# Kernel tuning notes

Measured on AMD Instinct MI355X. Metric: run time of the kernel, lower is better.

## Reference

```python
import jax, jax.numpy as jnp
import numpy as np

B, N, D, H = 8, 1024, 512, 8
DK = D // H  # key_dim == val_dim == 64
LN_EPS = 1e-5


def setup_inputs() -> dict:
    key = jax.random.key(0)
    ks = jax.random.split(key, 16)
    stdv = 1.0 / np.sqrt(D)
    u = lambda k, shape, s: jax.random.uniform(k, shape, jnp.float32, -s, s)
    inp = {
        'q': jax.random.normal(ks[0], (B, N, D), jnp.float32),
        'mask': jax.random.uniform(ks[1], (B, N, N)) < 0.1,  # True = masked out
        # eps1 is torch.zeros in the source (never re-initialized); use small
        'eps1': jax.random.normal(ks[2], (D, D), jnp.float32) * 0.03,
        # 3 MLP layers, stacked on leading axis. Linear: y = x @ W.T + b
        'U_w': u(ks[3], (3, D, D), stdv), 'U_b': u(ks[4], (3, D), stdv),
        'V_w': u(ks[5], (3, D, D), stdv), 'V_b': u(ks[6], (3, D), stdv),
        'ln_g': jnp.ones((3, D), jnp.float32), 'ln_b': jnp.zeros((3, D), jnp.float32),
        'W_query': u(ks[7], (H, D, DK), 1.0 / np.sqrt(DK)),
        'W_key':   u(ks[8], (H, D, DK), 1.0 / np.sqrt(DK)),
        'W_val':   u(ks[9], (H, D, DK), 1.0 / np.sqrt(DK)),
        'W_out':   u(ks[10], (H, DK, D), stdv),
    }
    return inp


def _layer_norm(x, g, b):
    mu = jnp.mean(x, axis=-1, keepdims=True)
    var = jnp.mean(jnp.square(x - mu), axis=-1, keepdims=True)
    return (x - mu) * jax.lax.rsqrt(var + LN_EPS) * g + b


def _mlp_layer(x, Uw, Ub, Vw, Vb, g, b):
    # U1 -> (identity maxpool k=1) -> V1 -> LayerNorm -> ReLU -> residual
    y = x @ Uw.T + Ub
    y = y @ Vw.T + Vb
    y = _layer_norm(y, g, b)
    return x + jax.nn.relu(y)


def reference(q, mask, eps1, U_w, U_b, V_w, V_b, ln_g, ln_b,
              W_query, W_key, W_val, W_out):
    nf = 1.0 / np.sqrt(DK)  # norm_factor; applied to BOTH Q and K as in source
    h = q
    for l in range(3):
        h = _mlp_layer(h @ eps1, U_w[l], U_b[l], V_w[l], V_b[l], ln_g[l], ln_b[l])
    # per-head projections: (H,B,N,DK)
    Q = jnp.einsum('bqd,hdk->hbqk', q, W_query) * nf
    K = jnp.einsum('bgd,hdk->hbgk', h, W_key) * nf
    V = jnp.einsum('bgd,hdk->hbgk', h, W_val)
    scores = jnp.einsum('hbqk,hbgk->hbqg', Q, K)  # (H,B,N,N)
    scores = jnp.where(mask[None], -1e10, scores)
    attn = jax.nn.softmax(scores, axis=-1)
    heads = jnp.einsum('hbqg,hbgv->hbqv', attn, V)
    out = jnp.einsum('hbqv,hvd->bqd', heads, W_out)  # (B,N,D)
    return out
```

## Files before the change

kernel.cpp:

```cpp
#include <hip/hip_runtime.h>

typedef __attribute__((ext_vector_type(8))) short bhalf8;
typedef __attribute__((ext_vector_type(4))) short bhalf4;
typedef __attribute__((ext_vector_type(4))) float f32x4;

__device__ __forceinline__ ushort f2bf(float f) {
  unsigned u = __builtin_bit_cast(unsigned, f);
  unsigned r = u + 0x7fffu + ((u >> 16) & 1u);
  return (ushort)(r >> 16);
}

__device__ __forceinline__ void gld16(const ushort* g, ushort* l) {
  __builtin_amdgcn_global_load_lds((const __attribute__((address_space(1))) void*)g,
                                   (__attribute__((address_space(3))) void*)l, 16, 0, 0);
}

__global__ __launch_bounds__(256) void prep_kernel(
    const float* __restrict__ q, const int* __restrict__ mask,
    const float* __restrict__ eps1, const float* __restrict__ U_w,
    const float* __restrict__ V_w, const float* __restrict__ Wq,
    const float* __restrict__ Wk, const float* __restrict__ Wv,
    const float* __restrict__ Wo, const float* __restrict__ U_b,
    const float* __restrict__ V_b,
    ushort* __restrict__ qb, unsigned long long* __restrict__ minv,
    ushort* __restrict__ uwb, ushort* __restrict__ vwb,
    ushort* __restrict__ e1b, ushort* __restrict__ e1t,
    ushort* __restrict__ wqkv, ushort* __restrict__ wot,
    float* __restrict__ cvec) {
  int i = blockIdx.x * 256 + threadIdx.x;
  if (i < 4194304) {
    qb[i] = f2bf(q[i]);
  } else if (i < 12582912) {
    int j = i - 4194304;
    unsigned long long bb = __ballot(mask[j] != 0);
    if ((threadIdx.x & 63) == 0) {
      int b = j >> 20, qq = (j >> 10) & 1023, g = j & 1023;
      minv[((size_t)b * 16 + (g >> 6)) * 1024 + qq] = ~bb;
    }
  } else if (i < 13369344) {
    int j = i - 12582912;
    uwb[j] = f2bf(U_w[j]);
  } else if (i < 14155776) {
    int j = i - 13369344;
    vwb[j] = f2bf(V_w[j]);
  } else if (i < 14417920) {
    int j = i - 14155776;
    e1b[j] = f2bf(eps1[j]);
  } else if (i < 14680064) {
    int j = i - 14417920; int n = j >> 9, k = j & 511;
    e1t[j] = f2bf(eps1[k * 512 + n]);
  } else if (i < 15466496) {
    int j = i - 14680064; int n = j >> 9, d = j & 511;
    const float* W = (n < 512) ? Wq : (n < 1024 ? Wk : Wv);
    float sc = (n < 512) ? 0.02255252509f : 1.0f;
    int nl = n & 511;
    wqkv[j] = f2bf(W[((nl >> 6) * 512 + d) * 64 + (nl & 63)] * sc);
  } else if (i < 15728640) {
    int j = i - 15466496; int d = j >> 9, hv = j & 511;
    wot[j] = f2bf(Wo[hv * 512 + d]);
  } else {
    int j = i - 15728640;
    int idx = j >> 6, ln = j & 63;
    int l = idx >> 9;
    const float* vr = V_w + (size_t)idx * 512 + ln * 8;
    const float* ur = U_b + l * 512 + ln * 8;
    float s = 0;
#pragma unroll
    for (int t = 0; t < 8; t++) s += vr[t] * ur[t];
#pragma unroll
    for (int off = 1; off < 64; off <<= 1) s += __shfl_xor(s, off, 64);
    if (ln == 0) cvec[idx] = s + V_b[idx];
  }
}

template <int BN>
__global__ __launch_bounds__(256) void gemm_nt(
    const ushort* __restrict__ A0, const ushort* __restrict__ A1,
    const ushort* __restrict__ Bt0, const ushort* __restrict__ Bt1,
    int bsplit, int mstride, int M, int K,
    ushort* __restrict__ Oa, const float* __restrict__ ba, int ca,
    ushort* __restrict__ Ob, const float* __restrict__ bb2, int cb,
    ushort* __restrict__ Oc, const float* __restrict__ bc, int cc) {
  __shared__ ushort As[128 * 32];
  __shared__ ushort Bs[BN * 32];
  int tid = threadIdx.x;
  int wave = tid >> 6, lane = tid & 63;
  int quad = lane >> 4, col = lane & 15;
  int m0 = blockIdx.x * 128, n0 = blockIdx.y * BN;
  const ushort* A = (A1 && n0 >= 512) ? A1 : A0;
  const ushort* Bp = ((n0 < bsplit) ? Bt0 + (size_t)n0 * K
                                    : Bt1 + (size_t)(n0 - bsplit) * K) +
                     (size_t)(m0 >> 9) * mstride;
  constexpr int NI = BN / 32;
  int wm = (BN == 128) ? (wave >> 1) * 64 : (wave & 1) * 64;
  int wn = (BN == 128) ? (wave & 1) * 64 : (wave >> 1) * 32;
  f32x4 acc[4][NI] = {};
  int srow = wave * 16 + (lane >> 2);
  int skc = (lane & 3) * 8;
  const ushort* gA0 = A + (size_t)(m0 + srow) * K + skc;
  const ushort* gA1 = gA0 + (size_t)64 * K;
  const ushort* gB0 = Bp + (size_t)srow * K + skc;
  const ushort* gB1 = gB0 + (size_t)64 * K;
  ushort* lA0 = &As[wave * 16 * 32];
  ushort* lA1 = &As[(64 + wave * 16) * 32];
  ushort* lB0 = &Bs[wave * 16 * 32];
  ushort* lB1 = (BN == 128) ? &Bs[(64 + wave * 16) * 32] : nullptr;

  gld16(gA0, lA0);
  gld16(gA1, lA1);
  gld16(gB0, lB0);
  if (BN == 128) gld16(gB1, lB1);

  for (int k0 = 0; k0 < K; k0 += 32) {
    __syncthreads();
    bhalf8 af[4], bg[NI];
#pragma unroll
    for (int i = 0; i < 4; i++)
      af[i] = *(bhalf8*)&As[(wm + i * 16 + col) * 32 + quad * 8];
#pragma unroll
    for (int i = 0; i < NI; i++)
      bg[i] = *(bhalf8*)&Bs[(wn + i * 16 + col) * 32 + quad * 8];
    __syncthreads();
    if (k0 + 32 < K) {
      gld16(gA0 + k0 + 32, lA0);
      gld16(gA1 + k0 + 32, lA1);
      gld16(gB0 + k0 + 32, lB0);
      if (BN == 128) gld16(gB1 + k0 + 32, lB1);
    }
#pragma unroll
    for (int mi = 0; mi < 4; mi++)
#pragma unroll
      for (int ni = 0; ni < NI; ni++)
        acc[mi][ni] = __builtin_amdgcn_mfma_f32_16x16x32_bf16(af[mi], bg[ni], acc[mi][ni], 0, 0, 0);
  }

  int reg = n0 >> 9;
  ushort* O = (reg == 0) ? Oa : (reg == 1 ? Ob : Oc);
  const float* bs = (reg == 0) ? ba : (reg == 1 ? bb2 : bc);
  int code = (reg == 0) ? ca : (reg == 1 ? cb : cc);
#pragma unroll
  for (int mi = 0; mi < 4; mi++)
#pragma unroll
    for (int ni = 0; ni < NI; ni++) {
      int cn = n0 + wn + ni * 16 + col;
      int cnl = cn & 511;
      int cmb = m0 + wm + mi * 16 + quad * 4;
      float bv = bs ? bs[cnl] : 0.f;
      if (code == 2) {
        int bhh = (cmb >> 10) * 8 + (cnl >> 6);
        size_t base = ((size_t)bhh * 64 + ((cmb & 1023) >> 4)) * 1024 +
                      (size_t)((cnl >> 5) & 1) * 512 + (size_t)(cmb & 15) * 32 + (cnl & 31);
#pragma unroll
        for (int r = 0; r < 4; r++)
          O[base + r * 32] = f2bf(acc[mi][ni][r] + bv);
      } else if (code == 3) {
        int bhh = (cmb >> 10) * 8 + (cnl >> 6);
        size_t base = ((size_t)bhh * 64 + ((cmb & 1023) >> 4)) * 1024 +
                      (size_t)(cnl & 63) * 16 + (cmb & 15);
        ushort4 pk;
        pk.x = f2bf(acc[mi][ni][0] + bv);
        pk.y = f2bf(acc[mi][ni][1] + bv);
        pk.z = f2bf(acc[mi][ni][2] + bv);
        pk.w = f2bf(acc[mi][ni][3] + bv);
        *(ushort4*)&O[base] = pk;
      } else if (code == 1) {
        float* Ff = (float*)O;
#pragma unroll
        for (int r = 0; r < 4; r++)
          Ff[(size_t)(cmb + r) * 512 + cnl] = acc[mi][ni][r] + bv;
      } else {
#pragma unroll
        for (int r = 0; r < 4; r++)
          O[(size_t)(cmb + r) * 512 + cnl] = f2bf(acc[mi][ni][r] + bv);
      }
    }
}

__global__ __launch_bounds__(256) void ln_kernel(
    const float* __restrict__ z, const ushort* __restrict__ tb,
    const float* __restrict__ lgam, const float* __restrict__ lbet,
    ushort* __restrict__ hb) {
  int row = blockIdx.x * 4 + (threadIdx.x >> 6);
  int lane = threadIdx.x & 63;
  int cbase = lane * 8;
  const float* zr = z + (size_t)row * 512 + cbase;
  float x[8];
  *(float4*)&x[0] = *(const float4*)zr;
  *(float4*)&x[4] = *(const float4*)(zr + 4);
  float sum = 0;
#pragma unroll
  for (int i = 0; i < 8; i++) sum += x[i];
#pragma unroll
  for (int off = 1; off < 64; off <<= 1) sum += __shfl_xor(sum, off, 64);
  float mu = sum * (1.f / 512.f);
  float vs = 0;
#pragma unroll
  for (int i = 0; i < 8; i++) { float d = x[i] - mu; vs += d * d; }
#pragma unroll
  for (int off = 1; off < 64; off <<= 1) vs += __shfl_xor(vs, off, 64);
  float rstd = rsqrtf(vs * (1.f / 512.f) + 1e-5f);
  uint4 tr = *(const uint4*)&tb[(size_t)row * 512 + cbase];
  float tv[8];
  {
    const unsigned* u = (const unsigned*)&tr;
#pragma unroll
    for (int w = 0; w < 4; w++) {
      tv[2 * w] = __builtin_bit_cast(float, u[w] << 16);
      tv[2 * w + 1] = __builtin_bit_cast(float, u[w] & 0xFFFF0000u);
    }
  }
  ushort outv[8];
#pragma unroll
  for (int i = 0; i < 8; i++) {
    float val = (x[i] - mu) * rstd * lgam[cbase + i] + lbet[cbase + i];
    outv[i] = f2bf(tv[i] + fmaxf(val, 0.f));
  }
  *(uint4*)&hb[(size_t)row * 512 + cbase] = *(uint4*)outv;
}

struct KVb { bhalf8 k[4]; bhalf4 v[8]; };

__device__ __forceinline__ void ldkv(KVb& d, const ushort* kp, const ushort* vp) {
  d.k[0] = *(const bhalf8*)kp;
  d.k[1] = *(const bhalf8*)(kp + 512);
  d.k[2] = *(const bhalf8*)(kp + 1024);
  d.k[3] = *(const bhalf8*)(kp + 1536);
#pragma unroll
  for (int i = 0; i < 8; i++) d.v[i] = *(const bhalf4*)(vp + i * 256);
}

__device__ __forceinline__ void attn_step(const KVb& kv, unsigned long long m,
                                          int bs, int quad, bhalf8 bq0, bhalf8 bq1,
                                          f32x4* o, float& lsum) {
  unsigned shq = (unsigned)(m >> (bs + quad * 4));
#pragma unroll
  for (int gt = 0; gt < 2; ++gt) {
    f32x4 s = {};
    s = __builtin_amdgcn_mfma_f32_16x16x32_bf16(kv.k[2 * gt], bq0, s, 0, 0, 0);
    s = __builtin_amdgcn_mfma_f32_16x16x32_bf16(kv.k[2 * gt + 1], bq1, s, 0, 0, 0);
    unsigned pu[4];
#pragma unroll
    for (int r = 0; r < 4; ++r) {
      const int pos = gt * 16 + r;
      unsigned keep = (unsigned)((int)(shq << (31 - pos)) >> 31);
      pu[r] = __builtin_bit_cast(unsigned, __builtin_amdgcn_exp2f(s[r])) & keep;
      lsum += __builtin_bit_cast(float, pu[r]);
    }
    uint2 pp;
    pp.x = ((pu[0] + 0x8000u) >> 16) | (((pu[1] + 0x8000u) >> 16) << 16);
    pp.y = ((pu[2] + 0x8000u) >> 16) | (((pu[3] + 0x8000u) >> 16) << 16);
    bhalf4 bp = __builtin_bit_cast(bhalf4, pp);
#pragma unroll
    for (int vt = 0; vt < 4; ++vt)
      o[vt] = __builtin_amdgcn_mfma_f32_16x16x16bf16_1k(kv.v[gt * 4 + vt], bp, o[vt], 0, 0, 0);
  }
}

__global__ __launch_bounds__(256, 4) void attn_kernel(
    const ushort* __restrict__ QtT, const ushort* __restrict__ KtT,
    const ushort* __restrict__ VtT, const unsigned long long* __restrict__ minv,
    ushort* __restrict__ Op) {
  int bh = blockIdx.x;
  int b = bh >> 3, h = bh & 7;
  int tid = threadIdx.x, w = tid >> 6, lane = tid & 63;
  int quad = lane >> 4, col = lane & 15;
  int qt = blockIdx.y * 4 + w;
  const ushort* Kt = KtT + (size_t)bh * 65536 + col * 32 + quad * 8;
  const ushort* Vt = VtT + (size_t)bh * 65536 + col * 16 + quad * 4;
  const ushort* Qt = QtT + (size_t)bh * 65536 + col * 32 + quad * 8;
  bhalf8 bq0 = *(const bhalf8*)(Qt + (size_t)qt * 1024);
  bhalf8 bq1 = *(const bhalf8*)(Qt + (size_t)qt * 1024 + 512);
  f32x4 o[4] = {};
  float lsum = 0.f;
  const unsigned long long* mb = minv + (size_t)b * 16384 + qt * 16 + col;

  KVb A, Bv;
  unsigned long long mcur = mb[0], mnxt = 0;
  ldkv(A, Kt, Vt);
  for (int p = 0; p < 30; p += 2) {
    ldkv(Bv, Kt + (size_t)(p + 1) * 2048, Vt + (size_t)(p + 1) * 2048);
    mnxt = mb[((p >> 1) + 1) * 1024];
    attn_step(A, mcur, 0, quad, bq0, bq1, o, lsum);
    ldkv(A, Kt + (size_t)(p + 2) * 2048, Vt + (size_t)(p + 2) * 2048);
    attn_step(Bv, mcur, 32, quad, bq0, bq1, o, lsum);
    mcur = mnxt;
  }
  ldkv(Bv, Kt + (size_t)31 * 2048, Vt + (size_t)31 * 2048);
  attn_step(A, mcur, 0, quad, bq0, bq1, o, lsum);
  attn_step(Bv, mcur, 32, quad, bq0, bq1, o, lsum);

  lsum += __shfl_xor(lsum, 16, 64);
  lsum += __shfl_xor(lsum, 32, 64);
  float rl = __builtin_amdgcn_rcpf(lsum);
  int q = qt * 16 + col;
#pragma unroll
  for (int vt = 0; vt < 4; ++vt) {
    ushort4 pk;
    pk.x = f2bf(o[vt][0] * rl);
    pk.y = f2bf(o[vt][1] * rl);
    pk.z = f2bf(o[vt][2] * rl);
    pk.w = f2bf(o[vt][3] * rl);
    *(ushort4*)&Op[(size_t)(b * 1024 + q) * 512 + h * 64 + vt * 16 + quad * 4] = pk;
  }
}

extern "C" void kernel_launch(void* const* d_in, const int* in_sizes, int n_in,
                              void* d_out, int out_size, void* d_ws, size_t ws_size,
                              hipStream_t stream) {
  const float* q    = (const float*)d_in[0];
  const int*   mask = (const int*)d_in[1];
  const float* eps1 = (const float*)d_in[2];
  const float* U_w  = (const float*)d_in[3];
  const float* U_b  = (const float*)d_in[4];
  const float* V_w  = (const float*)d_in[5];
  const float* V_b  = (const float*)d_in[6];
  const float* ln_g = (const float*)d_in[7];
  const float* ln_b = (const float*)d_in[8];
  const float* Wq   = (const float*)d_in[9];
  const float* Wk   = (const float*)d_in[10];
  const float* Wv   = (const float*)d_in[11];
  const float* Wo   = (const float*)d_in[12];
  float* out = (float*)d_out;

  char* ws = (char*)d_ws;
  auto carve = [&](size_t bytes) { char* p = ws; ws += bytes; return p; };
  ushort* qb   = (ushort*)carve(8388608);
  ushort* uwb  = (ushort*)carve(1572864);
  ushort* vwb  = (ushort*)carve(1572864);
  ushort* e1b  = (ushort*)carve(524288);
  ushort* e1t  = (ushort*)carve(524288);
  ushort* wqkv = (ushort*)carve(1572864);
  ushort* wot  = (ushort*)carve(524288);
  ushort* A1b  = (ushort*)carve(1572864);
  ushort* Gtb  = (ushort*)carve(1572864);
  float*  cvec = (float*)carve(6144);
  unsigned long long* minv = (unsigned long long*)carve(1048576);
  ushort* tb   = (ushort*)carve(8388608);
  float*  zf   = (float*)carve(16777216);
  ushort* hb   = (ushort*)carve(8388608);
  ushort* Qtt  = (ushort*)carve(8388608);
  ushort* Ktt  = (ushort*)carve(8388608);
  ushort* Vtt  = (ushort*)carve(8388608);
  ushort* Ob   = (ushort*)carve(8388608);
  const int BIG = 1 << 30;

  prep_kernel<<<61824, 256, 0, stream>>>(q, mask, eps1, U_w, V_w, Wq, Wk, Wv, Wo,
                                         U_b, V_b, qb, minv, uwb, vwb, e1b, e1t,
                                         wqkv, wot, cvec);
  gemm_nt<128><<<dim3(4, 12), 256, 0, stream>>>(
      e1b, nullptr, uwb, nullptr, BIG, 0, 512, 512,
      A1b, nullptr, 0, A1b + 262144, nullptr, 0, A1b + 524288, nullptr, 0);
  gemm_nt<64><<<dim3(12, 8), 256, 0, stream>>>(
      vwb, nullptr, A1b, nullptr, BIG, 262144, 1536, 512,
      Gtb, nullptr, 0, nullptr, nullptr, 0, nullptr, nullptr, 0);
  const ushort* hsrc = qb;
  for (int l = 0; l < 3; l++) {
    gemm_nt<128><<<dim3(64, 8), 256, 0, stream>>>(
        hsrc, nullptr, e1t, Gtb + l * 262144, 512, 0, 8192, 512,
        tb, nullptr, 0, (ushort*)zf, cvec + l * 512, 1, nullptr, nullptr, 0);
    ln_kernel<<<2048, 256, 0, stream>>>(zf, tb, ln_g + l * 512, ln_b + l * 512, hb);
    hsrc = hb;
  }
  gemm_nt<128><<<dim3(64, 12), 256, 0, stream>>>(
      qb, hb, wqkv, nullptr, BIG, 0, 8192, 512,
      Qtt, nullptr, 2, Ktt, nullptr, 2, Vtt, nullptr, 3);
  attn_kernel<<<dim3(64, 16), 256, 0, stream>>>(Qtt, Ktt, Vtt, minv, Ob);
  gemm_nt<64><<<dim3(64, 8), 256, 0, stream>>>(
      Ob, nullptr, wot, nullptr, BIG, 0, 8192, 512,
      (ushort*)out, nullptr, 1, nullptr, nullptr, 0, nullptr, nullptr, 0);
}
```

Before: 332.4 us.

## Stage K/V tiles through double-buffered LDS shared across attention waves

The attention kernel used to have each wave load its K and V fragments directly from global memory. Now the block cooperatively copies each 64-key chunk of K and V into a double-buffered shared-memory area using global_load_lds, and every wave reads its MFMA fragments from there. The aim is to cut redundant global/L2 traffic, since all four waves in a block share the same K/V, and to overlap the next chunk's copy with compute. The cost is two __syncthreads per iteration and 32 KB of LDS per block, which may limit occupancy and add barrier stalls.

```diff
diff --git a/kernel.cpp b/kernel.cpp
--- a/kernel.cpp
+++ b/kernel.cpp
@@ -218,76 +218,82 @@
   *(uint4*)&hb[(size_t)row * 512 + cbase] = *(uint4*)outv;
 }
 
-struct KVb { bhalf8 k[4]; bhalf4 v[8]; };
-
-__device__ __forceinline__ void ldkv(KVb& d, const ushort* kp, const ushort* vp) {
-  d.k[0] = *(const bhalf8*)kp;
-  d.k[1] = *(const bhalf8*)(kp + 512);
-  d.k[2] = *(const bhalf8*)(kp + 1024);
-  d.k[3] = *(const bhalf8*)(kp + 1536);
-#pragma unroll
-  for (int i = 0; i < 8; i++) d.v[i] = *(const bhalf4*)(vp + i * 256);
-}
-
-__device__ __forceinline__ void attn_step(const KVb& kv, unsigned long long m,
-                                          int bs, int quad, bhalf8 bq0, bhalf8 bq1,
-                                          f32x4* o, float& lsum) {
-  unsigned shq = (unsigned)(m >> (bs + quad * 4));
-#pragma unroll
-  for (int gt = 0; gt < 2; ++gt) {
-    f32x4 s = {};
-    s = __builtin_amdgcn_mfma_f32_16x16x32_bf16(kv.k[2 * gt], bq0, s, 0, 0, 0);
-    s = __builtin_amdgcn_mfma_f32_16x16x32_bf16(kv.k[2 * gt + 1], bq1, s, 0, 0, 0);
-    unsigned pu[4];
-#pragma unroll
-    for (int r = 0; r < 4; ++r) {
-      const int pos = gt * 16 + r;
-      unsigned keep = (unsigned)((int)(shq << (31 - pos)) >> 31);
-      pu[r] = __builtin_bit_cast(unsigned, __builtin_amdgcn_exp2f(s[r])) & keep;
-      lsum += __builtin_bit_cast(float, pu[r]);
-    }
-    uint2 pp;
-    pp.x = ((pu[0] + 0x8000u) >> 16) | (((pu[1] + 0x8000u) >> 16) << 16);
-    pp.y = ((pu[2] + 0x8000u) >> 16) | (((pu[3] + 0x8000u) >> 16) << 16);
-    bhalf4 bp = __builtin_bit_cast(bhalf4, pp);
-#pragma unroll
-    for (int vt = 0; vt < 4; ++vt)
-      o[vt] = __builtin_amdgcn_mfma_f32_16x16x16bf16_1k(kv.v[gt * 4 + vt], bp, o[vt], 0, 0, 0);
-  }
-}
-
 __global__ __launch_bounds__(256, 4) void attn_kernel(
     const ushort* __restrict__ QtT, const ushort* __restrict__ KtT,
     const ushort* __restrict__ VtT, const unsigned long long* __restrict__ minv,
     ushort* __restrict__ Op) {
+  __shared__ ushort lds[16384];
   int bh = blockIdx.x;
   int b = bh >> 3, h = bh & 7;
   int tid = threadIdx.x, w = tid >> 6, lane = tid & 63;
   int quad = lane >> 4, col = lane & 15;
   int qt = blockIdx.y * 4 + w;
-  const ushort* Kt = KtT + (size_t)bh * 65536 + col * 32 + quad * 8;
-  const ushort* Vt = VtT + (size_t)bh * 65536 + col * 16 + quad * 4;
+  const ushort* Kg = KtT + (size_t)bh * 65536 + tid * 8;
+  const ushort* Vg = VtT + (size_t)bh * 65536 + tid * 8;
   const ushort* Qt = QtT + (size_t)bh * 65536 + col * 32 + quad * 8;
   bhalf8 bq0 = *(const bhalf8*)(Qt + (size_t)qt * 1024);
   bhalf8 bq1 = *(const bhalf8*)(Qt + (size_t)qt * 1024 + 512);
   f32x4 o[4] = {};
   float lsum = 0.f;
   const unsigned long long* mb = minv + (size_t)b * 16384 + qt * 16 + col;
-
-  KVb A, Bv;
+  int kread = col * 32 + quad * 8;
+  int vread = col * 16 + quad * 4;
+
+  {
+    ushort* lk = &lds[w * 512];
+    ushort* lv = &lds[4096 + w * 512];
+    gld16(Kg, lk); gld16(Kg + 2048, lk + 2048);
+    gld16(Vg, lv); gld16(Vg + 2048, lv + 2048);
+  }
   unsigned long long mcur = mb[0], mnxt = 0;
-  ldkv(A, Kt, Vt);
-  for (int p = 0; p < 30; p += 2) {
-    ldkv(Bv, Kt + (size_t)(p + 1) * 2048, Vt + (size_t)(p + 1) * 2048);
-    mnxt = mb[((p >> 1) + 1) * 1024];
-    attn_step(A, mcur, 0, quad, bq0, bq1, o, lsum);
-    ldkv(A, Kt + (size_t)(p + 2) * 2048, Vt + (size_t)(p + 2) * 2048);
-    attn_step(Bv, mcur, 32, quad, bq0, bq1, o, lsum);
+
+  for (int p = 0; p < 16; ++p) {
+    int cb = (p & 1) * 8192;
+    __syncthreads();
+    bhalf8 ak[4][2];
+    bhalf4 av[4][4];
+#pragma unroll
+    for (int gt = 0; gt < 4; ++gt) {
+      ak[gt][0] = *(const bhalf8*)&lds[cb + gt * 1024 + kread];
+      ak[gt][1] = *(const bhalf8*)&lds[cb + gt * 1024 + 512 + kread];
+#pragma unroll
+      for (int vt = 0; vt < 4; ++vt)
+        av[gt][vt] = *(const bhalf4*)&lds[cb + 4096 + gt * 1024 + vt * 256 + vread];
+    }
+    __syncthreads();
+    if (p < 15) {
+      int nb = (cb ^ 8192);
+      ushort* lk = &lds[nb + w * 512];
+      ushort* lv = &lds[nb + 4096 + w * 512];
+      const ushort* gk = Kg + (size_t)(p + 1) * 4096;
+      const ushort* gv = Vg + (size_t)(p + 1) * 4096;
+      gld16(gk, lk); gld16(gk + 2048, lk + 2048);
+      gld16(gv, lv); gld16(gv + 2048, lv + 2048);
+      mnxt = mb[(size_t)(p + 1) * 1024];
+    }
+#pragma unroll
+    for (int gt = 0; gt < 4; ++gt) {
+      f32x4 s = {};
+      s = __builtin_amdgcn_mfma_f32_16x16x32_bf16(ak[gt][0], bq0, s, 0, 0, 0);
+      s = __builtin_amdgcn_mfma_f32_16x16x32_bf16(ak[gt][1], bq1, s, 0, 0, 0);
+      unsigned shq = (unsigned)(mcur >> (gt * 16 + quad * 4));
+      unsigned pu[4];
+#pragma unroll
+      for (int r = 0; r < 4; ++r) {
+        unsigned keep = (unsigned)((int)(shq << (31 - r)) >> 31);
+        pu[r] = __builtin_bit_cast(unsigned, __builtin_amdgcn_exp2f(s[r])) & keep;
+        lsum += __builtin_bit_cast(float, pu[r]);
+      }
+      uint2 pp;
+      pp.x = ((pu[0] + 0x8000u) >> 16) | (((pu[1] + 0x8000u) >> 16) << 16);
+      pp.y = ((pu[2] + 0x8000u) >> 16) | (((pu[3] + 0x8000u) >> 16) << 16);
+      bhalf4 bp = __builtin_bit_cast(bhalf4, pp);
+#pragma unroll
+      for (int vt = 0; vt < 4; ++vt)
+        o[vt] = __builtin_amdgcn_mfma_f32_16x16x16bf16_1k(av[gt][vt], bp, o[vt], 0, 0, 0);
+    }
     mcur = mnxt;
   }
-  ldkv(Bv, Kt + (size_t)31 * 2048, Vt + (size_t)31 * 2048);
-  attn_step(A, mcur, 0, quad, bq0, bq1, o, lsum);
-  attn_step(Bv, mcur, 32, quad, bq0, bq1, o, lsum);
 
   lsum += __shfl_xor(lsum, 16, 64);
   lsum += __shfl_xor(lsum, 32, 64);
```

New measurement: 309.8 us. -6.8%, faster.
